# Kernel tuning notes

Measured on AMD Instinct MI355X. Metric: run time of the kernel, lower is better.

The kernel has to match this reference:

```python
import jax, jax.numpy as jnp
import numpy as np

BN_EPS = 1e-5
LEAKY_SLOPE = 0.01

N_TOTAL, FEAT_DIM = 100000, 128
N_BATCH, K = 50000, 16
EMBED_DIM = 128


def setup_inputs() -> dict:
    key = jax.random.key(0)
    k1, k2, k3 = jax.random.split(key, 3)
    raw_features = jax.random.normal(k1, (N_TOTAL, FEAT_DIM), dtype=jnp.float32)
    weight = jax.random.normal(k2, (FEAT_DIM, EMBED_DIM), dtype=jnp.float32) * (1.0 / np.sqrt(FEAT_DIM))
    gamma = jnp.ones((EMBED_DIM,), dtype=jnp.float32)
    beta = jnp.zeros((EMBED_DIM,), dtype=jnp.float32)
    neigh_idx = jax.random.randint(k3, (N_BATCH, K), 0, N_TOTAL, dtype=jnp.int64)
    return {"raw_features": raw_features, "weight": weight, "gamma": gamma,
            "beta": beta, "neigh_idx": neigh_idx}


def reference(raw_features, weight, gamma, beta, neigh_idx):
    # Mean aggregation over sampled neighbors: [N_BATCH, K, F] -> [N_BATCH, F]
    neigh_feats = jnp.mean(raw_features[neigh_idx], axis=1)
    # Dense transform: [N_BATCH, EMBED_DIM]
    x = neigh_feats @ weight
    # BatchNorm1d (training mode: batch statistics, biased variance)
    mean = jnp.mean(x, axis=0)
    var = jnp.var(x, axis=0)
    x = (x - mean) * jax.lax.rsqrt(var + BN_EPS) * gamma + beta
    # LeakyReLU (default negative_slope=0.01)
    return jnp.where(x >= 0, x, LEAKY_SLOPE * x)
```

## Files before the change

### kernel.cpp

```cpp
#include <hip/hip_runtime.h>
#include <hip/hip_bf16.h>
#include <hip/hip_cooperative_groups.h>

namespace cg = cooperative_groups;


#define NTOTAL 100000
#define FEAT   128
#define NB     50000
#define KNEI   16
#define NTILES (NB / 16)
#define ZTILES (NTOTAL / 16)
#define NSLOT  8
#define TMAX   4

#define OFF_PSTAT 0
#define OFF_ZB    8192
#define OFF_XB    (8192 + 25600000)
#define WS_NEEDED (OFF_XB + 12800000)

typedef float f32x4 __attribute__((ext_vector_type(4)));
typedef short bf16x8 __attribute__((ext_vector_type(8)));

__device__ __forceinline__ unsigned short f2bf(float f) {
    union { float f; unsigned u; } v; v.f = f;
    unsigned r = v.u + 0x7FFF + ((v.u >> 16) & 1);
    return (unsigned short)(r >> 16);
}

#define WT_LD 136
#define A_LD  136
#define SMEM_BYTES 39168

__global__ __launch_bounds__(256, 4) void enc_all(
    const float* __restrict__ raw, const float* __restrict__ W,
    const float* __restrict__ gamma, const float* __restrict__ beta,
    const int* __restrict__ idx, float* __restrict__ out,
    unsigned short* __restrict__ Zb, float* __restrict__ pstats)
{
    __shared__ __align__(16) char smem[SMEM_BYTES];
    unsigned short* sWt = (unsigned short*)smem;
    unsigned short* sA  = (unsigned short*)(smem + 34816);
    int*   sidx = (int*)smem;
    float* sRed = (float*)(smem + 1024);
    float* sSS  = (float*)smem;

    cg::grid_group grid = cg::this_grid();
    const int t = threadIdx.x;

    if (blockIdx.x == 0) {
        #pragma unroll
        for (int i = 0; i < NSLOT; ++i) pstats[t + i * 256] = 0.f;
    }

    #pragma unroll
    for (int i = 0; i < 16; ++i) {
        int e = t + i * 256;
        float4 w4 = ((const float4*)W)[e];
        int li = e * 4;
        int k = li >> 7, n = li & 127;
        sWt[(n + 0) * WT_LD + k] = f2bf(w4.x);
        sWt[(n + 1) * WT_LD + k] = f2bf(w4.y);
        sWt[(n + 2) * WT_LD + k] = f2bf(w4.z);
        sWt[(n + 3) * WT_LD + k] = f2bf(w4.w);
    }

    const int lane = t & 63;
    const int wv = t >> 6;
    const int ln = lane & 15;
    const int qd = lane >> 4;
    const int c2 = t & 15;
    const int g  = t >> 4;
    const int n0 = wv * 32 + ln, n1 = n0 + 16;

    for (int tile = blockIdx.x; tile < ZTILES; tile += gridDim.x) {
        const int r0 = tile * 16;
        __syncthreads();
        {
            const float4* rp = (const float4*)&raw[(size_t)(r0 + g) * FEAT + c2 * 8];
            float4 x0 = rp[0], x1 = rp[1];
            uint4 b;
            b.x = (unsigned)f2bf(x0.x) | ((unsigned)f2bf(x0.y) << 16);
            b.y = (unsigned)f2bf(x0.z) | ((unsigned)f2bf(x0.w) << 16);
            b.z = (unsigned)f2bf(x1.x) | ((unsigned)f2bf(x1.y) << 16);
            b.w = (unsigned)f2bf(x1.z) | ((unsigned)f2bf(x1.w) << 16);
            *(uint4*)&sA[g * A_LD + c2 * 8] = b;
        }
        __syncthreads();

        f32x4 acc0 = {0.f, 0.f, 0.f, 0.f}, acc1 = {0.f, 0.f, 0.f, 0.f};
        #pragma unroll
        for (int kt = 0; kt < 4; ++kt) {
            const int k0 = kt * 32 + qd * 8;
            bf16x8 a  = *(const bf16x8*)&sA[ln * A_LD + k0];
            bf16x8 b0 = *(const bf16x8*)&sWt[n0 * WT_LD + k0];
            bf16x8 b1 = *(const bf16x8*)&sWt[n1 * WT_LD + k0];
            acc0 = __builtin_amdgcn_mfma_f32_16x16x32_bf16(a, b0, acc0, 0, 0, 0);
            acc1 = __builtin_amdgcn_mfma_f32_16x16x32_bf16(a, b1, acc1, 0, 0, 0);
        }

        #pragma unroll
        for (int ri = 0; ri < 4; ++ri) {
            const int row = r0 + qd * 4 + ri;
            Zb[row * FEAT + n0] = f2bf(acc0[ri]);
            Zb[row * FEAT + n1] = f2bf(acc1[ri]);
        }
    }
    grid.sync();

    uint4 xr0 = {0,0,0,0}, xr1 = {0,0,0,0}, xr2 = {0,0,0,0}, xr3 = {0,0,0,0};
    float s1[8], s2[8];
    #pragma unroll
    for (int j = 0; j < 8; ++j) { s1[j] = 0.f; s2[j] = 0.f; }

    #pragma unroll
    for (int tt = 0; tt < TMAX; ++tt) {
        const int tile = blockIdx.x + tt * gridDim.x;
        if (tile < NTILES) {
            __syncthreads();
            sidx[t] = idx[tile * 16 * KNEI + t];
            __syncthreads();

            const int* ip = &sidx[g * KNEI];
            uint4 v[16];
            #pragma unroll
            for (int k = 0; k < KNEI; ++k)
                v[k] = *(const uint4*)&Zb[(size_t)ip[k] * FEAT + c2 * 8];
            __builtin_amdgcn_sched_barrier(0);

            float a[8];
            #pragma unroll
            for (int j = 0; j < 8; ++j) a[j] = 0.f;
            #pragma unroll
            for (int k = 0; k < KNEI; ++k) {
                a[0] += __uint_as_float(v[k].x << 16);
                a[1] += __uint_as_float(v[k].x & 0xFFFF0000u);
                a[2] += __uint_as_float(v[k].y << 16);
                a[3] += __uint_as_float(v[k].y & 0xFFFF0000u);
                a[4] += __uint_as_float(v[k].z << 16);
                a[5] += __uint_as_float(v[k].z & 0xFFFF0000u);
                a[6] += __uint_as_float(v[k].w << 16);
                a[7] += __uint_as_float(v[k].w & 0xFFFF0000u);
            }
            #pragma unroll
            for (int j = 0; j < 8; ++j) a[j] *= 0.0625f;

            #pragma unroll
            for (int j = 0; j < 8; ++j) { s1[j] += a[j]; s2[j] += a[j] * a[j]; }

            uint4 b;
            b.x = (unsigned)f2bf(a[0]) | ((unsigned)f2bf(a[1]) << 16);
            b.y = (unsigned)f2bf(a[2]) | ((unsigned)f2bf(a[3]) << 16);
            b.z = (unsigned)f2bf(a[4]) | ((unsigned)f2bf(a[5]) << 16);
            b.w = (unsigned)f2bf(a[6]) | ((unsigned)f2bf(a[7]) << 16);
            if (tt == 0) xr0 = b;
            else if (tt == 1) xr1 = b;
            else if (tt == 2) xr2 = b;
            else xr3 = b;
        }
    }

    #pragma unroll
    for (int j = 0; j < 8; ++j) {
        s1[j] += __shfl_down(s1[j], 32); s1[j] += __shfl_down(s1[j], 16);
        s2[j] += __shfl_down(s2[j], 32); s2[j] += __shfl_down(s2[j], 16);
    }
    __syncthreads();
    if (lane < 16) {
        #pragma unroll
        for (int j = 0; j < 8; ++j) {
            sRed[wv * 256 + c2 * 8 + j]       = s1[j];
            sRed[wv * 256 + 128 + c2 * 8 + j] = s2[j];
        }
    }
    __syncthreads();
    {
        float s = sRed[t] + sRed[256 + t] + sRed[512 + t] + sRed[768 + t];
        atomicAdd(&pstats[(blockIdx.x & (NSLOT - 1)) * 256 + t], s);
    }
    grid.sync();

    if (t < FEAT) {
        float a1 = 0.f, a2 = 0.f;
        #pragma unroll
        for (int sl = 0; sl < NSLOT; ++sl) {
            a1 += pstats[sl * 256 + t];
            a2 += pstats[sl * 256 + 128 + t];
        }
        float mean = a1 * (1.0f / NB);
        float var = a2 * (1.0f / NB) - mean * mean;
        float sc = gamma[t] * rsqrtf(var + 1e-5f);
        sSS[t] = sc;
        sSS[FEAT + t] = beta[t] - mean * sc;
    }
    __syncthreads();

    const int f8 = c2 * 8;
    const float4 sc0 = *(const float4*)&sSS[f8], sc1 = *(const float4*)&sSS[f8 + 4];
    const float4 sh0 = *(const float4*)&sSS[FEAT + f8], sh1 = *(const float4*)&sSS[FEAT + f8 + 4];

    #pragma unroll
    for (int tt = 0; tt < TMAX; ++tt) {
        const int tile = blockIdx.x + tt * gridDim.x;
        if (tile < NTILES) {
            uint4 v = (tt == 0) ? xr0 : (tt == 1) ? xr1 : (tt == 2) ? xr2 : xr3;
            float4 r0, r1; float y;
            y = __uint_as_float(v.x << 16)        * sc0.x + sh0.x; r0.x = (y >= 0.f) ? y : 0.01f * y;
            y = __uint_as_float(v.x & 0xFFFF0000u)* sc0.y + sh0.y; r0.y = (y >= 0.f) ? y : 0.01f * y;
            y = __uint_as_float(v.y << 16)        * sc0.z + sh0.z; r0.z = (y >= 0.f) ? y : 0.01f * y;
            y = __uint_as_float(v.y & 0xFFFF0000u)* sc0.w + sh0.w; r0.w = (y >= 0.f) ? y : 0.01f * y;
            y = __uint_as_float(v.z << 16)        * sc1.x + sh1.x; r1.x = (y >= 0.f) ? y : 0.01f * y;
            y = __uint_as_float(v.z & 0xFFFF0000u)* sc1.y + sh1.y; r1.y = (y >= 0.f) ? y : 0.01f * y;
            y = __uint_as_float(v.w << 16)        * sc1.z + sh1.z; r1.z = (y >= 0.f) ? y : 0.01f * y;
            y = __uint_as_float(v.w & 0xFFFF0000u)* sc1.w + sh1.w; r1.w = (y >= 0.f) ? y : 0.01f * y;
            float4* op = (float4*)&out[(size_t)(tile * 16 + g) * FEAT + f8];
            op[0] = r0; op[1] = r1;
        }
    }
}

__global__ __launch_bounds__(256, 4) void enc_zgemm(
    const float* __restrict__ raw, const float* __restrict__ W,
    unsigned short* __restrict__ Zb, float* __restrict__ pstats)
{
    __shared__ unsigned short sWt[128 * WT_LD];
    __shared__ unsigned short sA[16 * A_LD];
    const int t = threadIdx.x;
    if (blockIdx.x == 0) {
        #pragma unroll
        for (int i = 0; i < NSLOT; ++i) pstats[t + i * 256] = 0.f;
    }
    #pragma unroll
    for (int i = 0; i < 16; ++i) {
        int e = t + i * 256;
        float4 w4 = ((const float4*)W)[e];
        int li = e * 4;
        int k = li >> 7, n = li & 127;
        sWt[(n + 0) * WT_LD + k] = f2bf(w4.x);
        sWt[(n + 1) * WT_LD + k] = f2bf(w4.y);
        sWt[(n + 2) * WT_LD + k] = f2bf(w4.z);
        sWt[(n + 3) * WT_LD + k] = f2bf(w4.w);
    }
    const int lane = t & 63;
    const int wv = t >> 6, ln = lane & 15, qd = lane >> 4;
    const int c2 = t & 15, g = t >> 4;
    const int n0 = wv * 32 + ln, n1 = n0 + 16;
    for (int tile = blockIdx.x; tile < ZTILES; tile += gridDim.x) {
        const int r0 = tile * 16;
        __syncthreads();
        {
            const float4* rp = (const float4*)&raw[(size_t)(r0 + g) * FEAT + c2 * 8];
            float4 x0 = rp[0], x1 = rp[1];
            uint4 b;
            b.x = (unsigned)f2bf(x0.x) | ((unsigned)f2bf(x0.y) << 16);
            b.y = (unsigned)f2bf(x0.z) | ((unsigned)f2bf(x0.w) << 16);
            b.z = (unsigned)f2bf(x1.x) | ((unsigned)f2bf(x1.y) << 16);
            b.w = (unsigned)f2bf(x1.z) | ((unsigned)f2bf(x1.w) << 16);
            *(uint4*)&sA[g * A_LD + c2 * 8] = b;
        }
        __syncthreads();
        f32x4 acc0 = {0.f, 0.f, 0.f, 0.f}, acc1 = {0.f, 0.f, 0.f, 0.f};
        #pragma unroll
        for (int kt = 0; kt < 4; ++kt) {
            const int k0 = kt * 32 + qd * 8;
            bf16x8 a  = *(const bf16x8*)&sA[ln * A_LD + k0];
            bf16x8 b0 = *(const bf16x8*)&sWt[n0 * WT_LD + k0];
            bf16x8 b1 = *(const bf16x8*)&sWt[n1 * WT_LD + k0];
            acc0 = __builtin_amdgcn_mfma_f32_16x16x32_bf16(a, b0, acc0, 0, 0, 0);
            acc1 = __builtin_amdgcn_mfma_f32_16x16x32_bf16(a, b1, acc1, 0, 0, 0);
        }
        #pragma unroll
        for (int ri = 0; ri < 4; ++ri) {
            const int row = r0 + qd * 4 + ri;
            Zb[row * FEAT + n0] = f2bf(acc0[ri]);
            Zb[row * FEAT + n1] = f2bf(acc1[ri]);
        }
    }
}

__global__ __launch_bounds__(256, 4) void enc_gather(
    const unsigned short* __restrict__ Zb, const int* __restrict__ idx,
    unsigned short* __restrict__ xb, float* __restrict__ pstats)
{
    __shared__ int sidx[256];
    __shared__ float sRed[4 * 256];
    const int t = threadIdx.x;
    const int i0 = blockIdx.x * 16;
    sidx[t] = idx[i0 * KNEI + t];
    __syncthreads();
    const int g = t >> 4, c2 = t & 15;
    const int* ip = &sidx[g * KNEI];
    uint4 v[16];
    #pragma unroll
    for (int k = 0; k < KNEI; ++k)
        v[k] = *(const uint4*)&Zb[(size_t)ip[k] * FEAT + c2 * 8];
    __builtin_amdgcn_sched_barrier(0);
    float a[8];
    #pragma unroll
    for (int j = 0; j < 8; ++j) a[j] = 0.f;
    #pragma unroll
    for (int k = 0; k < KNEI; ++k) {
        a[0] += __uint_as_float(v[k].x << 16);
        a[1] += __uint_as_float(v[k].x & 0xFFFF0000u);
        a[2] += __uint_as_float(v[k].y << 16);
        a[3] += __uint_as_float(v[k].y & 0xFFFF0000u);
        a[4] += __uint_as_float(v[k].z << 16);
        a[5] += __uint_as_float(v[k].z & 0xFFFF0000u);
        a[6] += __uint_as_float(v[k].w << 16);
        a[7] += __uint_as_float(v[k].w & 0xFFFF0000u);
    }
    #pragma unroll
    for (int j = 0; j < 8; ++j) a[j] *= 0.0625f;
    {
        uint4 b;
        b.x = (unsigned)f2bf(a[0]) | ((unsigned)f2bf(a[1]) << 16);
        b.y = (unsigned)f2bf(a[2]) | ((unsigned)f2bf(a[3]) << 16);
        b.z = (unsigned)f2bf(a[4]) | ((unsigned)f2bf(a[5]) << 16);
        b.w = (unsigned)f2bf(a[6]) | ((unsigned)f2bf(a[7]) << 16);
        *(uint4*)&xb[(size_t)(i0 + g) * FEAT + c2 * 8] = b;
    }
    float q[8];
    #pragma unroll
    for (int j = 0; j < 8; ++j) q[j] = a[j] * a[j];
    #pragma unroll
    for (int j = 0; j < 8; ++j) {
        a[j] += __shfl_down(a[j], 32); a[j] += __shfl_down(a[j], 16);
        q[j] += __shfl_down(q[j], 32); q[j] += __shfl_down(q[j], 16);
    }
    const int lane = t & 63, wv = t >> 6;
    if (lane < 16) {
        #pragma unroll
        for (int j = 0; j < 8; ++j) {
            sRed[wv * 256 + c2 * 8 + j]       = a[j];
            sRed[wv * 256 + 128 + c2 * 8 + j] = q[j];
        }
    }
    __syncthreads();
    float s = sRed[t] + sRed[256 + t] + sRed[512 + t] + sRed[768 + t];
    atomicAdd(&pstats[(blockIdx.x & (NSLOT - 1)) * 256 + t], s);
}

__global__ __launch_bounds__(256) void enc_bn(
    const unsigned short* __restrict__ xb, float* __restrict__ out,
    const float* __restrict__ pstats,
    const float* __restrict__ gamma, const float* __restrict__ beta)
{
    __shared__ float sScale[FEAT], sShift[FEAT];
    const int t = threadIdx.x;
    if (t < FEAT) {
        float s1 = 0.f, s2 = 0.f;
        #pragma unroll
        for (int sl = 0; sl < NSLOT; ++sl) {
            s1 += pstats[sl * 256 + t];
            s2 += pstats[sl * 256 + 128 + t];
        }
        float mean = s1 * (1.0f / NB);
        float var = s2 * (1.0f / NB) - mean * mean;
        float sc = gamma[t] * rsqrtf(var + 1e-5f);
        sScale[t] = sc;
        sShift[t] = beta[t] - mean * sc;
    }
    __syncthreads();
    const int f8 = (t & 15) * 8;
    const float4 sc0 = *(const float4*)&sScale[f8], sc1 = *(const float4*)&sScale[f8 + 4];
    const float4 sh0 = *(const float4*)&sShift[f8], sh1 = *(const float4*)&sShift[f8 + 4];
    const uint4* x4 = (const uint4*)xb;
    float4* o4 = (float4*)out;
    const int total8 = NB * FEAT / 8;
    for (int e = blockIdx.x * 256 + t; e < total8; e += gridDim.x * 256) {
        uint4 v = x4[e];
        float4 r0, r1; float y;
        y = __uint_as_float(v.x << 16)        * sc0.x + sh0.x; r0.x = (y >= 0.f) ? y : 0.01f * y;
        y = __uint_as_float(v.x & 0xFFFF0000u)* sc0.y + sh0.y; r0.y = (y >= 0.f) ? y : 0.01f * y;
        y = __uint_as_float(v.y << 16)        * sc0.z + sh0.z; r0.z = (y >= 0.f) ? y : 0.01f * y;
        y = __uint_as_float(v.y & 0xFFFF0000u)* sc0.w + sh0.w; r0.w = (y >= 0.f) ? y : 0.01f * y;
        y = __uint_as_float(v.z << 16)        * sc1.x + sh1.x; r1.x = (y >= 0.f) ? y : 0.01f * y;
        y = __uint_as_float(v.z & 0xFFFF0000u)* sc1.y + sh1.y; r1.y = (y >= 0.f) ? y : 0.01f * y;
        y = __uint_as_float(v.w << 16)        * sc1.z + sh1.z; r1.z = (y >= 0.f) ? y : 0.01f * y;
        y = __uint_as_float(v.w & 0xFFFF0000u)* sc1.w + sh1.w; r1.w = (y >= 0.f) ? y : 0.01f * y;
        o4[e * 2] = r0; o4[e * 2 + 1] = r1;
    }
}

__global__ __launch_bounds__(256, 4) void enc_gemm_f(
    const float* __restrict__ raw, const float* __restrict__ W,
    const int* __restrict__ idx, float* __restrict__ out,
    float* __restrict__ gstats)
{
    __shared__ unsigned short sWt[128 * WT_LD];
    __shared__ unsigned short sA[16 * A_LD];
    __shared__ int sidx[256];
    const int t = threadIdx.x;
    #pragma unroll 4
    for (int i = 0; i < 64; ++i) {
        int e = t + i * 256;
        int f = e >> 7, n = e & 127;
        sWt[n * WT_LD + f] = f2bf(W[e]);
    }
    const int lane = t & 63, wv = t >> 6, ln = lane & 15, qd = lane >> 4;
    const int c = t & 31, g = t >> 5;
    const int n0 = wv * 32 + ln, n1 = n0 + 16;
    float s1a = 0.f, s2a = 0.f, s1b = 0.f, s2b = 0.f;
    const float4* raw4 = (const float4*)raw;
    for (int tile = blockIdx.x; tile < NTILES; tile += gridDim.x) {
        const int i0 = tile * 16;
        __syncthreads();
        sidx[t] = idx[i0 * KNEI + t];
        __syncthreads();
        #pragma unroll
        for (int rr = 0; rr < 2; ++rr) {
            const int r = g * 2 + rr;
            const int* ip = &sidx[r * KNEI];
            float4 acc = {0.f, 0.f, 0.f, 0.f};
            #pragma unroll
            for (int k = 0; k < KNEI; ++k) {
                float4 v = raw4[(size_t)ip[k] * 32 + c];
                acc.x += v.x; acc.y += v.y; acc.z += v.z; acc.w += v.w;
            }
            ushort4 b;
            b.x = f2bf(acc.x * 0.0625f); b.y = f2bf(acc.y * 0.0625f);
            b.z = f2bf(acc.z * 0.0625f); b.w = f2bf(acc.w * 0.0625f);
            *(ushort4*)&sA[r * A_LD + c * 4] = b;
        }
        __syncthreads();
        f32x4 acc0 = {0.f, 0.f, 0.f, 0.f}, acc1 = {0.f, 0.f, 0.f, 0.f};
        #pragma unroll
        for (int kt = 0; kt < 4; ++kt) {
            const int k0 = kt * 32 + qd * 8;
            bf16x8 a  = *(const bf16x8*)&sA[ln * A_LD + k0];
            bf16x8 b0 = *(const bf16x8*)&sWt[n0 * WT_LD + k0];
            bf16x8 b1 = *(const bf16x8*)&sWt[n1 * WT_LD + k0];
            acc0 = __builtin_amdgcn_mfma_f32_16x16x32_bf16(a, b0, acc0, 0, 0, 0);
            acc1 = __builtin_amdgcn_mfma_f32_16x16x32_bf16(a, b1, acc1, 0, 0, 0);
        }
        #pragma unroll
        for (int ri = 0; ri < 4; ++ri) {
            const int row = i0 + qd * 4 + ri;
            float v0 = acc0[ri], v1 = acc1[ri];
            out[row * FEAT + n0] = v0;
            out[row * FEAT + n1] = v1;
            s1a += v0; s2a += v0 * v0;
            s1b += v1; s2b += v1 * v1;
        }
    }
    s1a += __shfl_down(s1a, 32); s1a += __shfl_down(s1a, 16);
    s2a += __shfl_down(s2a, 32); s2a += __shfl_down(s2a, 16);
    s1b += __shfl_down(s1b, 32); s1b += __shfl_down(s1b, 16);
    s2b += __shfl_down(s2b, 32); s2b += __shfl_down(s2b, 16);
    if (qd == 0) {
        atomicAdd(&gstats[n0], s1a);
        atomicAdd(&gstats[FEAT + n0], s2a);
        atomicAdd(&gstats[n1], s1b);
        atomicAdd(&gstats[FEAT + n1], s2b);
    }
}

__global__ __launch_bounds__(256) void enc_bn_f(
    float* __restrict__ out, const float* __restrict__ gstats,
    const float* __restrict__ gamma, const float* __restrict__ beta)
{
    __shared__ float sScale[FEAT], sShift[FEAT];
    const int t = threadIdx.x;
    if (t < FEAT) {
        float s1 = gstats[t], s2 = gstats[FEAT + t];
        float mean = s1 * (1.0f / NB);
        float var = s2 * (1.0f / NB) - mean * mean;
        float sc = gamma[t] * rsqrtf(var + 1e-5f);
        sScale[t] = sc;
        sShift[t] = beta[t] - mean * sc;
    }
    __syncthreads();
    const int f4 = (t & 31) * 4;
    const float4 sc = *(const float4*)&sScale[f4];
    const float4 sh = *(const float4*)&sShift[f4];
    const int total4 = NB * FEAT / 4;
    float4* o4 = (float4*)out;
    for (int e = blockIdx.x * 256 + t; e < total4; e += gridDim.x * 256) {
        float4 v = o4[e];
        float4 r; float y;
        y = v.x * sc.x + sh.x; r.x = (y >= 0.f) ? y : 0.01f * y;
        y = v.y * sc.y + sh.y; r.y = (y >= 0.f) ? y : 0.01f * y;
        y = v.z * sc.z + sh.z; r.z = (y >= 0.f) ? y : 0.01f * y;
        y = v.w * sc.w + sh.w; r.w = (y >= 0.f) ? y : 0.01f * y;
        o4[e] = r;
    }
}

extern "C" void kernel_launch(void* const* d_in, const int* in_sizes, int n_in,
                              void* d_out, int out_size, void* d_ws, size_t ws_size,
                              hipStream_t stream) {
    const float* raw   = (const float*)d_in[0];
    const float* W     = (const float*)d_in[1];
    const float* gamma = (const float*)d_in[2];
    const float* beta  = (const float*)d_in[3];
    const int*   idx   = (const int*)d_in[4];
    float* out = (float*)d_out;

    char* ws = (char*)d_ws;
    float* pstats      = (float*)(ws + OFF_PSTAT);
    unsigned short* Zb = (unsigned short*)(ws + OFF_ZB);
    unsigned short* xb = (unsigned short*)(ws + OFF_XB);

    static int coopGrid = -1;
    if (coopGrid < 0) {
        int g = 0, dev = 0, occ = 0;
        hipDeviceProp_t prop;
        if (hipGetDevice(&dev) == hipSuccess &&
            hipGetDeviceProperties(&prop, dev) == hipSuccess &&
            prop.cooperativeLaunch &&
            hipOccupancyMaxActiveBlocksPerMultiprocessor(&occ, enc_all, 256, 0) == hipSuccess &&
            occ > 0) {
            g = occ * prop.multiProcessorCount;
            if (g > 1024) g = 1024;
        }
        if (g * TMAX < NTILES) g = 0;
        coopGrid = g;
    }

    if (ws_size >= WS_NEEDED && coopGrid > 0) {
        void* args[] = { (void*)&raw, (void*)&W, (void*)&gamma, (void*)&beta,
                         (void*)&idx, (void*)&out, (void*)&Zb, (void*)&pstats };
        hipError_t e = hipLaunchCooperativeKernel(enc_all, dim3(coopGrid), dim3(256),
                                                  args, 0u, stream);
        if (e == hipSuccess) return;
        coopGrid = 0;
    }

    if (ws_size >= WS_NEEDED) {
        enc_zgemm<<<1042, 256, 0, stream>>>(raw, W, Zb, pstats);
        enc_gather<<<NTILES, 256, 0, stream>>>(Zb, idx, xb, pstats);
        enc_bn<<<1024, 256, 0, stream>>>(xb, out, pstats, gamma, beta);
    } else {
        float* gstats = (float*)(ws + OFF_PSTAT);
        hipMemsetAsync(gstats, 0, 2 * FEAT * sizeof(float), stream);
        enc_gemm_f<<<1024, 256, 0, stream>>>(raw, W, idx, out, gstats);
        enc_bn_f<<<1024, 256, 0, stream>>>(out, gstats, gamma, beta);
    }
}
```

Baseline: 152.0 us.

## Split cooperative kernel into GEMM launch plus gather/BN kernel with custom barrier

Replaces the single cooperative kernel, which used two grid.sync calls, with a plain GEMM kernel followed by a gather+BN kernel. The second kernel uses a hand-rolled atomic-counter spin barrier in workspace memory, and the kernel boundary now serves as the first sync. The gather grid can grow to 2048 blocks with up to 5 tiles per block, which allows more occupancy. The aim is to avoid cooperative launch overhead and the heavier grid-wide sync. The spin barrier assumes every block of the gather kernel is co-resident, or it can deadlock.

```diff
diff --git a/kernel.cpp b/kernel.cpp
--- a/kernel.cpp
+++ b/kernel.cpp
@@ -1,8 +1,5 @@
 #include <hip/hip_runtime.h>
 #include <hip/hip_bf16.h>
-#include <hip/hip_cooperative_groups.h>
-
-namespace cg = cooperative_groups;
 
 
 #define NTOTAL 100000
@@ -12,11 +9,12 @@
 #define NTILES (NB / 16)
 #define ZTILES (NTOTAL / 16)
 #define NSLOT  8
-#define TMAX   4
+#define TMAX   5
 
 #define OFF_PSTAT 0
-#define OFF_ZB    8192
-#define OFF_XB    (8192 + 25600000)
+#define OFF_BAR   8192
+#define OFF_ZB    8320
+#define OFF_XB    (8320 + 25600000)
 #define WS_NEEDED (OFF_XB + 12800000)
 
 typedef float f32x4 __attribute__((ext_vector_type(4)));
@@ -30,27 +28,21 @@
 
 #define WT_LD 136
 #define A_LD  136
-#define SMEM_BYTES 39168
-
-__global__ __launch_bounds__(256, 4) void enc_all(
+
+__global__ __launch_bounds__(256, 4) void enc_zgemm(
     const float* __restrict__ raw, const float* __restrict__ W,
-    const float* __restrict__ gamma, const float* __restrict__ beta,
-    const int* __restrict__ idx, float* __restrict__ out,
-    unsigned short* __restrict__ Zb, float* __restrict__ pstats)
-{
-    __shared__ __align__(16) char smem[SMEM_BYTES];
-    unsigned short* sWt = (unsigned short*)smem;
-    unsigned short* sA  = (unsigned short*)(smem + 34816);
-    int*   sidx = (int*)smem;
-    float* sRed = (float*)(smem + 1024);
-    float* sSS  = (float*)smem;
-
-    cg::grid_group grid = cg::this_grid();
+    unsigned short* __restrict__ Zb, float* __restrict__ pstats,
+    unsigned* __restrict__ bar)
+{
+    __shared__ unsigned short sWt[128 * WT_LD];
+    __shared__ unsigned short sA[16 * A_LD];
+
     const int t = threadIdx.x;
 
     if (blockIdx.x == 0) {
         #pragma unroll
         for (int i = 0; i < NSLOT; ++i) pstats[t + i * 256] = 0.f;
+        if (t < 32) bar[t] = 0u;
     }
 
     #pragma unroll
@@ -106,16 +98,31 @@
             Zb[row * FEAT + n1] = f2bf(acc1[ri]);
         }
     }
-    grid.sync();
-
-    uint4 xr0 = {0,0,0,0}, xr1 = {0,0,0,0}, xr2 = {0,0,0,0}, xr3 = {0,0,0,0};
+}
+
+__global__ __launch_bounds__(256, 4) void enc_gather_bn(
+    const unsigned short* __restrict__ Zb, const int* __restrict__ idx,
+    const float* __restrict__ gamma, const float* __restrict__ beta,
+    float* __restrict__ out, float* __restrict__ pstats,
+    unsigned* __restrict__ bar)
+{
+    __shared__ int sidx[256];
+    __shared__ float sRed[4 * 256];
+    __shared__ float sSS[2 * FEAT];
+
+    const int t = threadIdx.x;
+    const int G = gridDim.x;
+    const int g = t >> 4, c2 = t & 15;
+    const int lane = t & 63, wv = t >> 6;
+
+    uint4 xr0 = {0,0,0,0}, xr1 = {0,0,0,0}, xr2 = {0,0,0,0}, xr3 = {0,0,0,0}, xr4 = {0,0,0,0};
     float s1[8], s2[8];
     #pragma unroll
     for (int j = 0; j < 8; ++j) { s1[j] = 0.f; s2[j] = 0.f; }
 
     #pragma unroll
     for (int tt = 0; tt < TMAX; ++tt) {
-        const int tile = blockIdx.x + tt * gridDim.x;
+        const int tile = blockIdx.x + tt * G;
         if (tile < NTILES) {
             __syncthreads();
             sidx[t] = idx[tile * 16 * KNEI + t];
@@ -156,7 +163,8 @@
             if (tt == 0) xr0 = b;
             else if (tt == 1) xr1 = b;
             else if (tt == 2) xr2 = b;
-            else xr3 = b;
+            else if (tt == 3) xr3 = b;
+            else xr4 = b;
         }
     }
 
@@ -178,14 +186,30 @@
         float s = sRed[t] + sRed[256 + t] + sRed[512 + t] + sRed[768 + t];
         atomicAdd(&pstats[(blockIdx.x & (NSLOT - 1)) * 256 + t], s);
     }
-    grid.sync();
+
+    __syncthreads();
+    if (t == 0) {
+        __threadfence();
+        unsigned arrived = __hip_atomic_fetch_add(&bar[0], 1u, __ATOMIC_ACQ_REL,
+                                                  __HIP_MEMORY_SCOPE_AGENT) + 1u;
+        if (arrived == (unsigned)G) {
+            __hip_atomic_store(&bar[1], 1u, __ATOMIC_RELEASE, __HIP_MEMORY_SCOPE_AGENT);
+        } else {
+            while (__hip_atomic_load(&bar[1], __ATOMIC_ACQUIRE,
+                                     __HIP_MEMORY_SCOPE_AGENT) == 0u)
+                __builtin_amdgcn_s_sleep(8);
+        }
+    }
+    __syncthreads();
 
     if (t < FEAT) {
         float a1 = 0.f, a2 = 0.f;
         #pragma unroll
         for (int sl = 0; sl < NSLOT; ++sl) {
-            a1 += pstats[sl * 256 + t];
-            a2 += pstats[sl * 256 + 128 + t];
+            a1 += __hip_atomic_load(&pstats[sl * 256 + t], __ATOMIC_RELAXED,
+                                    __HIP_MEMORY_SCOPE_AGENT);
+            a2 += __hip_atomic_load(&pstats[sl * 256 + 128 + t], __ATOMIC_RELAXED,
+                                    __HIP_MEMORY_SCOPE_AGENT);
         }
         float mean = a1 * (1.0f / NB);
         float var = a2 * (1.0f / NB) - mean * mean;
@@ -201,9 +225,10 @@
 
     #pragma unroll
     for (int tt = 0; tt < TMAX; ++tt) {
-        const int tile = blockIdx.x + tt * gridDim.x;
+        const int tile = blockIdx.x + tt * G;
         if (tile < NTILES) {
-            uint4 v = (tt == 0) ? xr0 : (tt == 1) ? xr1 : (tt == 2) ? xr2 : xr3;
+            uint4 v = (tt == 0) ? xr0 : (tt == 1) ? xr1 : (tt == 2) ? xr2
+                    : (tt == 3) ? xr3 : xr4;
             float4 r0, r1; float y;
             y = __uint_as_float(v.x << 16)        * sc0.x + sh0.x; r0.x = (y >= 0.f) ? y : 0.01f * y;
             y = __uint_as_float(v.x & 0xFFFF0000u)* sc0.y + sh0.y; r0.y = (y >= 0.f) ? y : 0.01f * y;
@@ -215,65 +240,6 @@
             y = __uint_as_float(v.w & 0xFFFF0000u)* sc1.w + sh1.w; r1.w = (y >= 0.f) ? y : 0.01f * y;
             float4* op = (float4*)&out[(size_t)(tile * 16 + g) * FEAT + f8];
             op[0] = r0; op[1] = r1;
-        }
-    }
-}
-
-__global__ __launch_bounds__(256, 4) void enc_zgemm(
-    const float* __restrict__ raw, const float* __restrict__ W,
-    unsigned short* __restrict__ Zb, float* __restrict__ pstats)
-{
-    __shared__ unsigned short sWt[128 * WT_LD];
-    __shared__ unsigned short sA[16 * A_LD];
-    const int t = threadIdx.x;
-    if (blockIdx.x == 0) {
-        #pragma unroll
-        for (int i = 0; i < NSLOT; ++i) pstats[t + i * 256] = 0.f;
-    }
-    #pragma unroll
-    for (int i = 0; i < 16; ++i) {
-        int e = t + i * 256;
-        float4 w4 = ((const float4*)W)[e];
-        int li = e * 4;
-        int k = li >> 7, n = li & 127;
-        sWt[(n + 0) * WT_LD + k] = f2bf(w4.x);
-        sWt[(n + 1) * WT_LD + k] = f2bf(w4.y);
-        sWt[(n + 2) * WT_LD + k] = f2bf(w4.z);
-        sWt[(n + 3) * WT_LD + k] = f2bf(w4.w);
-    }
-    const int lane = t & 63;
-    const int wv = t >> 6, ln = lane & 15, qd = lane >> 4;
-    const int c2 = t & 15, g = t >> 4;
-    const int n0 = wv * 32 + ln, n1 = n0 + 16;
-    for (int tile = blockIdx.x; tile < ZTILES; tile += gridDim.x) {
-        const int r0 = tile * 16;
-        __syncthreads();
-        {
-            const float4* rp = (const float4*)&raw[(size_t)(r0 + g) * FEAT + c2 * 8];
-            float4 x0 = rp[0], x1 = rp[1];
-            uint4 b;
-            b.x = (unsigned)f2bf(x0.x) | ((unsigned)f2bf(x0.y) << 16);
-            b.y = (unsigned)f2bf(x0.z) | ((unsigned)f2bf(x0.w) << 16);
-            b.z = (unsigned)f2bf(x1.x) | ((unsigned)f2bf(x1.y) << 16);
-            b.w = (unsigned)f2bf(x1.z) | ((unsigned)f2bf(x1.w) << 16);
-            *(uint4*)&sA[g * A_LD + c2 * 8] = b;
-        }
-        __syncthreads();
-        f32x4 acc0 = {0.f, 0.f, 0.f, 0.f}, acc1 = {0.f, 0.f, 0.f, 0.f};
-        #pragma unroll
-        for (int kt = 0; kt < 4; ++kt) {
-            const int k0 = kt * 32 + qd * 8;
-            bf16x8 a  = *(const bf16x8*)&sA[ln * A_LD + k0];
-            bf16x8 b0 = *(const bf16x8*)&sWt[n0 * WT_LD + k0];
-            bf16x8 b1 = *(const bf16x8*)&sWt[n1 * WT_LD + k0];
-            acc0 = __builtin_amdgcn_mfma_f32_16x16x32_bf16(a, b0, acc0, 0, 0, 0);
-            acc1 = __builtin_amdgcn_mfma_f32_16x16x32_bf16(a, b1, acc1, 0, 0, 0);
-        }
-        #pragma unroll
-        for (int ri = 0; ri < 4; ++ri) {
-            const int row = r0 + qd * 4 + ri;
-            Zb[row * FEAT + n0] = f2bf(acc0[ri]);
-            Zb[row * FEAT + n1] = f2bf(acc1[ri]);
         }
     }
 }
@@ -498,36 +464,30 @@
 
     char* ws = (char*)d_ws;
     float* pstats      = (float*)(ws + OFF_PSTAT);
+    unsigned* bar      = (unsigned*)(ws + OFF_BAR);
     unsigned short* Zb = (unsigned short*)(ws + OFF_ZB);
     unsigned short* xb = (unsigned short*)(ws + OFF_XB);
 
-    static int coopGrid = -1;
-    if (coopGrid < 0) {
-        int g = 0, dev = 0, occ = 0;
+    static int g2 = -1;
+    if (g2 < 0) {
+        int dev = 0, occ = 0, g = 0;
         hipDeviceProp_t prop;
         if (hipGetDevice(&dev) == hipSuccess &&
             hipGetDeviceProperties(&prop, dev) == hipSuccess &&
-            prop.cooperativeLaunch &&
-            hipOccupancyMaxActiveBlocksPerMultiprocessor(&occ, enc_all, 256, 0) == hipSuccess &&
+            hipOccupancyMaxActiveBlocksPerMultiprocessor(&occ, enc_gather_bn, 256, 0) == hipSuccess &&
             occ > 0) {
             g = occ * prop.multiProcessorCount;
-            if (g > 1024) g = 1024;
+            if (g > 2048) g = 2048;
         }
         if (g * TMAX < NTILES) g = 0;
-        coopGrid = g;
-    }
-
-    if (ws_size >= WS_NEEDED && coopGrid > 0) {
-        void* args[] = { (void*)&raw, (void*)&W, (void*)&gamma, (void*)&beta,
-                         (void*)&idx, (void*)&out, (void*)&Zb, (void*)&pstats };
-        hipError_t e = hipLaunchCooperativeKernel(enc_all, dim3(coopGrid), dim3(256),
-                                                  args, 0u, stream);
-        if (e == hipSuccess) return;
-        coopGrid = 0;
-    }
-
-    if (ws_size >= WS_NEEDED) {
-        enc_zgemm<<<1042, 256, 0, stream>>>(raw, W, Zb, pstats);
+        g2 = g;
+    }
+
+    if (ws_size >= WS_NEEDED && g2 > 0) {
+        enc_zgemm<<<1042, 256, 0, stream>>>(raw, W, Zb, pstats, bar);
+        enc_gather_bn<<<g2, 256, 0, stream>>>(Zb, idx, gamma, beta, out, pstats, bar);
+    } else if (ws_size >= WS_NEEDED) {
+        enc_zgemm<<<1042, 256, 0, stream>>>(raw, W, Zb, pstats, bar);
         enc_gather<<<NTILES, 256, 0, stream>>>(Zb, idx, xb, pstats);
         enc_bn<<<1024, 256, 0, stream>>>(xb, out, pstats, gamma, beta);
     } else {
```

Result: no change. 153.3 us (+0.9%).
